# Kernel tuning notes

Measured on AMD Instinct MI355X. Metric: run time of the kernel, lower is better.

The kernel has to match this reference:

```python
import jax, jax.numpy as jnp
import numpy as np

DIM = 1024
EPS = 1e-5

def layernorm(x, g, b):
    m = jnp.mean(x, axis=-1, keepdims=True)
    v = jnp.var(x, axis=-1, keepdims=True)
    return (x - m) / jnp.sqrt(v + EPS) * g + b

def setup_inputs() -> dict:
    key = jax.random.key(0)
    ks = jax.random.split(key, 12)
    B, L, D = 4, 2048, DIM
    s = 1.0 / np.sqrt(D)
    return {
        "q": jax.random.normal(ks[0], (B, L, D), jnp.float32),
        "k": jax.random.normal(ks[1], (B, L, D), jnp.float32),
        "v": jax.random.normal(ks[2], (B, L, D), jnp.float32),
        "gq": jnp.ones((D,), jnp.float32), "bq": jnp.zeros((D,), jnp.float32),
        "gk": jnp.ones((D,), jnp.float32), "bk": jnp.zeros((D,), jnp.float32),
        "gv": jnp.ones((D,), jnp.float32), "bv": jnp.zeros((D,), jnp.float32),
        "Wq": jax.random.uniform(ks[3], (D, D), jnp.float32, -s, s),
        "Wk": jax.random.uniform(ks[4], (D, D), jnp.float32, -s, s),
        "Wv": jax.random.uniform(ks[5], (D, D), jnp.float32, -s, s),
        "Wp": jax.random.uniform(ks[6], (D, D), jnp.float32, -s, s),
        "bp": jax.random.uniform(ks[7], (D,), jnp.float32, -s, s),
    }

def reference(q, k, v, gq, bq, gk, bk, gv, bv, Wq, Wk, Wv, Wp, bp):
    scale = DIM ** -0.5
    qn = layernorm(q, gq, bq) @ Wq.T  # [B,Q,D]
    kn = layernorm(k, gk, bk) @ Wk.T  # [B,K,D]
    vn = layernorm(v, gv, bv) @ Wv.T  # [B,K,D]
    attn = jnp.einsum('bqc,bkc->bqk', qn, kn)
    attn = jax.nn.relu(attn) * scale  # ReLU on raw scores, then scale (matches in-place *=)
    attn_mask = jax.nn.softmax(attn, axis=-1)
    out = jnp.einsum('bqk,bkc->bqc', attn_mask, vn)
    out = out @ Wp.T + bp
    return (attn, out)
```

## Files before the change

### kernel.cpp

```cpp
#include <hip/hip_runtime.h>


typedef __attribute__((ext_vector_type(8))) short short8v;
typedef __attribute__((ext_vector_type(4))) float f32x4;

#define DEVI __device__ __forceinline__

DEVI float b2f(unsigned short u) {
  union { unsigned int i; float f; } x;
  x.i = ((unsigned int)u) << 16;
  return x.f;
}
DEVI unsigned short f2b(float f) {
  union { float f; unsigned int i; } x;
  x.f = f;
  unsigned int r = x.i + 0x7fffu + ((x.i >> 16) & 1u);
  return (unsigned short)(r >> 16);
}

DEVI void async16(const unsigned short* g, unsigned short* l) {
  __builtin_amdgcn_global_load_lds(
      (const __attribute__((address_space(1))) void*)g,
      (__attribute__((address_space(3))) void*)l, 16, 0, 0);
}

__global__ void k_sniff(const unsigned short* __restrict__ wq, int* __restrict__ flag) {
  int tid = threadIdx.x;
  int bad = 0;
#pragma unroll
  for (int j = 0; j < 8; ++j) {
    float f = b2f(wq[tid * 8 + j]);
    bad |= (fabsf(f) > 0.0625f) ? 1 : 0;
  }
  unsigned long long m = __ballot(bad);
  if (tid == 0) *flag = (m == 0ull) ? 1 : 0;
}

struct CvtSrc { const void* p[11]; };

__global__ __launch_bounds__(256) void k_cvt(CvtSrc cs,
    unsigned short* __restrict__ wdst, unsigned short* __restrict__ vdst,
    const int* __restrict__ flag) {
  bool isbf = (*flag != 0);
  int bid = blockIdx.x;
  if (bid < 2048) {
    int s = bid >> 9;
    size_t inner = ((size_t)(bid & 511)) * 2048 + (size_t)threadIdx.x * 8;
    unsigned short* dst = wdst + (size_t)s * 1048576 + inner;
    if (isbf) {
      *(uint4*)dst = *(const uint4*)((const unsigned short*)cs.p[s] + inner);
    } else {
      const float* f = (const float*)cs.p[s] + inner;
      float4 a = *(const float4*)f;
      float4 b = *(const float4*)(f + 4);
      ushort4 o0 = { f2b(a.x), f2b(a.y), f2b(a.z), f2b(a.w) };
      ushort4 o1 = { f2b(b.x), f2b(b.y), f2b(b.z), f2b(b.w) };
      *(ushort4*)dst = o0;
      *(ushort4*)(dst + 4) = o1;
    }
  } else {
    size_t idx = ((size_t)(bid - 2048)) * 2048 + (size_t)threadIdx.x * 8;
    if (idx < 7168) {
      int vsel = (int)(idx >> 10);
      size_t pos = idx & 1023;
      unsigned short* dst = vdst + idx;
      if (isbf) {
        *(uint4*)dst = *(const uint4*)((const unsigned short*)cs.p[4 + vsel] + pos);
      } else {
        const float* f = (const float*)cs.p[4 + vsel] + pos;
        float4 a = *(const float4*)f;
        float4 b = *(const float4*)(f + 4);
        ushort4 o0 = { f2b(a.x), f2b(a.y), f2b(a.z), f2b(a.w) };
        ushort4 o1 = { f2b(b.x), f2b(b.y), f2b(b.z), f2b(b.w) };
        *(ushort4*)dst = o0;
        *(ushort4*)(dst + 4) = o1;
      }
    }
  }
}

__global__ __launch_bounds__(256) void k_ln(
    const void* __restrict__ q, const void* __restrict__ k, const void* __restrict__ v,
    const unsigned short* __restrict__ vecs, const int* __restrict__ flag,
    unsigned short* __restrict__ xn) {
  int row = blockIdx.x;
  int t = row >> 13;
  size_t r = (size_t)(row & 8191);
  const void* src = (t == 0) ? q : (t == 1) ? k : v;
  int tid = threadIdx.x;
  float x0, x1, x2, x3;
  if (*flag) {
    const unsigned short* p = (const unsigned short*)src + r * 1024 + (size_t)tid * 4;
    ushort4 pk = *(const ushort4*)p;
    x0 = b2f(pk.x); x1 = b2f(pk.y); x2 = b2f(pk.z); x3 = b2f(pk.w);
  } else {
    const float* p = (const float*)src + r * 1024 + (size_t)tid * 4;
    float4 pk = *(const float4*)p;
    x0 = pk.x; x1 = pk.y; x2 = pk.z; x3 = pk.w;
  }
  float s1 = x0 + x1 + x2 + x3;
  float s2 = x0 * x0 + x1 * x1 + x2 * x2 + x3 * x3;
  for (int off = 32; off > 0; off >>= 1) {
    s1 += __shfl_down(s1, off);
    s2 += __shfl_down(s2, off);
  }
  __shared__ float sh[8];
  if ((tid & 63) == 0) { sh[tid >> 6] = s1; sh[4 + (tid >> 6)] = s2; }
  __syncthreads();
  float m  = (sh[0] + sh[1] + sh[2] + sh[3]) * (1.0f / 1024.0f);
  float m2 = (sh[4] + sh[5] + sh[6] + sh[7]) * (1.0f / 1024.0f);
  float rstd = rsqrtf(m2 - m * m + 1e-5f);
  const unsigned short* g = vecs + t * 2048 + tid * 4;
  ushort4 gv = *(const ushort4*)g;
  ushort4 bb = *(const ushort4*)(g + 1024);
  ushort4 o;
  o.x = f2b((x0 - m) * rstd * b2f(gv.x) + b2f(bb.x));
  o.y = f2b((x1 - m) * rstd * b2f(gv.y) + b2f(bb.y));
  o.z = f2b((x2 - m) * rstd * b2f(gv.z) + b2f(bb.z));
  o.w = f2b((x3 - m) * rstd * b2f(gv.w) + b2f(bb.w));
  *(ushort4*)(xn + (size_t)row * 1024 + (size_t)tid * 4) = o;
}

__global__ __launch_bounds__(256) void k_softmax(const void* __restrict__ S,
    unsigned short* __restrict__ P, const int* __restrict__ flag) {
  size_t row = blockIdx.x;
  int tid = threadIdx.x;
  float v[8];
  if (*flag) {
    const unsigned short* s = (const unsigned short*)S + row * 2048 + (size_t)tid * 8;
    ushort4 a = *(const ushort4*)s;
    ushort4 b = *(const ushort4*)(s + 4);
    v[0] = b2f(a.x); v[1] = b2f(a.y); v[2] = b2f(a.z); v[3] = b2f(a.w);
    v[4] = b2f(b.x); v[5] = b2f(b.y); v[6] = b2f(b.z); v[7] = b2f(b.w);
  } else {
    const float* s = (const float*)S + row * 2048 + (size_t)tid * 8;
    float4 a = *(const float4*)s;
    float4 b = *(const float4*)(s + 4);
    v[0] = a.x; v[1] = a.y; v[2] = a.z; v[3] = a.w;
    v[4] = b.x; v[5] = b.y; v[6] = b.z; v[7] = b.w;
  }
  float mx = v[0];
#pragma unroll
  for (int j = 1; j < 8; ++j) mx = fmaxf(mx, v[j]);
  for (int off = 32; off > 0; off >>= 1) mx = fmaxf(mx, __shfl_down(mx, off));
  __shared__ float sh[8];
  if ((tid & 63) == 0) sh[tid >> 6] = mx;
  __syncthreads();
  mx = fmaxf(fmaxf(sh[0], sh[1]), fmaxf(sh[2], sh[3]));
  float sum = 0.f;
#pragma unroll
  for (int j = 0; j < 8; ++j) { v[j] = __expf(v[j] - mx); sum += v[j]; }
  for (int off = 32; off > 0; off >>= 1) sum += __shfl_down(sum, off);
  if ((tid & 63) == 0) sh[4 + (tid >> 6)] = sum;
  __syncthreads();
  float inv = 1.0f / (sh[4] + sh[5] + sh[6] + sh[7]);
  ushort4 o0 = { f2b(v[0] * inv), f2b(v[1] * inv), f2b(v[2] * inv), f2b(v[3] * inv) };
  ushort4 o1 = { f2b(v[4] * inv), f2b(v[5] * inv), f2b(v[6] * inv), f2b(v[7] * inv) };
  unsigned short* p = P + row * 2048 + (size_t)tid * 8;
  *(ushort4*)p = o0;
  *(ushort4*)(p + 4) = o1;
}

template <int EPI>
__global__ __launch_bounds__(256) void k_gemm(
    const unsigned short* __restrict__ A, const unsigned short* __restrict__ B,
    void* __restrict__ Cv, long long coff,
    int K, int lda, int ldb, int ldc, int ldct,
    long long sAb, long long sBb, long long sCb,
    float scale, const unsigned short* __restrict__ bias,
    const int* __restrict__ flag) {
  __shared__ __align__(16) unsigned short sA[128 * 32];
  __shared__ __align__(16) unsigned short sB[128 * 32];
  const unsigned short* Ab = A + (long long)blockIdx.z * sAb;
  const unsigned short* Bb = B + (long long)blockIdx.z * sBb;
  long long cbase = coff + (long long)blockIdx.z * sCb;
  int m0 = blockIdx.y * 128, n0 = blockIdx.x * 128;
  int tid = threadIdx.x;
  int lane = tid & 63;
  int w = tid >> 6;
  int wm = w & 1, wn = w >> 1;
  int l15 = lane & 15, quad = lane >> 4;

  int srow = w * 32 + (lane >> 2);
  int scol = ((lane & 3) ^ ((lane >> 3) & 3)) * 8;
  const unsigned short* gA0 = Ab + (size_t)(m0 + srow) * lda + scol;
  const unsigned short* gA1 = gA0 + (size_t)16 * lda;
  const unsigned short* gB0 = Bb + (size_t)(n0 + srow) * ldb + scol;
  const unsigned short* gB1 = gB0 + (size_t)16 * ldb;
  unsigned short* lA0 = &sA[w * 1024];
  unsigned short* lA1 = &sA[w * 1024 + 512];
  unsigned short* lB0 = &sB[w * 1024];
  unsigned short* lB1 = &sB[w * 1024 + 512];

  int swz = (quad ^ ((l15 >> 1) & 3)) * 8;
  const unsigned short* rA = &sA[(wm * 64 + l15) * 32 + swz];
  const unsigned short* rB = &sB[(wn * 64 + l15) * 32 + swz];

  f32x4 acc[4][4];
#pragma unroll
  for (int i = 0; i < 4; ++i)
#pragma unroll
    for (int j = 0; j < 4; ++j) acc[i][j] = (f32x4){0.f, 0.f, 0.f, 0.f};

  for (int k0 = 0; k0 < K; k0 += 32) {
    async16(gA0 + k0, lA0);
    async16(gA1 + k0, lA1);
    async16(gB0 + k0, lB0);
    async16(gB1 + k0, lB1);
    __syncthreads();
    short8v af[4], bf[4];
#pragma unroll
    for (int i = 0; i < 4; ++i) {
      af[i] = *(const short8v*)(rA + i * 512);
      bf[i] = *(const short8v*)(rB + i * 512);
    }
#pragma unroll
    for (int mt = 0; mt < 4; ++mt)
#pragma unroll
      for (int nt = 0; nt < 4; ++nt)
        acc[mt][nt] = __builtin_amdgcn_mfma_f32_16x16x32_bf16(af[mt], bf[nt], acc[mt][nt], 0, 0, 0);
    __syncthreads();
  }

  bool isbf = (EPI == 1 || EPI == 3) ? (*flag != 0) : true;
#pragma unroll
  for (int mt = 0; mt < 4; ++mt) {
    int mb = m0 + wm * 64 + mt * 16 + quad * 4;
#pragma unroll
    for (int nt = 0; nt < 4; ++nt) {
      int n = n0 + wn * 64 + nt * 16 + l15;
      f32x4 vc = acc[mt][nt];
      if (EPI == 2) {
        unsigned short* Ct = (unsigned short*)Cv + cbase;
        ushort4 o = { f2b(vc[0]), f2b(vc[1]), f2b(vc[2]), f2b(vc[3]) };
        *(ushort4*)&Ct[(size_t)n * ldct + mb] = o;
      } else if (EPI == 0) {
        unsigned short* C = (unsigned short*)Cv + cbase;
#pragma unroll
        for (int r2 = 0; r2 < 4; ++r2) C[(size_t)(mb + r2) * ldc + n] = f2b(vc[r2]);
      } else if (EPI == 1) {
        if (isbf) {
          unsigned short* C = (unsigned short*)Cv + cbase;
#pragma unroll
          for (int r2 = 0; r2 < 4; ++r2)
            C[(size_t)(mb + r2) * ldc + n] = f2b(fmaxf(vc[r2], 0.f) * scale);
        } else {
          float* C = (float*)Cv + cbase;
#pragma unroll
          for (int r2 = 0; r2 < 4; ++r2)
            C[(size_t)(mb + r2) * ldc + n] = fmaxf(vc[r2], 0.f) * scale;
        }
      } else {
        float bv2 = b2f(bias[n]);
        if (isbf) {
          unsigned short* C = (unsigned short*)Cv + cbase;
#pragma unroll
          for (int r2 = 0; r2 < 4; ++r2) C[(size_t)(mb + r2) * ldc + n] = f2b(vc[r2] + bv2);
        } else {
          float* C = (float*)Cv + cbase;
#pragma unroll
          for (int r2 = 0; r2 < 4; ++r2) C[(size_t)(mb + r2) * ldc + n] = vc[r2] + bv2;
        }
      }
    }
  }
}

static const size_t MB_ = 1024 * 1024;
static const size_t OFF_W   = 0;
static const size_t OFF_VEC = 8 * MB_;
static const size_t OFF_FLG = 8 * MB_ + 64 * 1024;
static const size_t OFF_XN  = 8 * MB_ + 128 * 1024;
static const size_t OFF_QN  = OFF_XN + 48 * MB_;
static const size_t OFF_KN  = OFF_QN + 16 * MB_;
static const size_t OFF_VNT = OFF_KN + 16 * MB_;
static const size_t OFF_P   = OFF_XN;
static const size_t OFF_O1  = OFF_XN + 32 * MB_;

extern "C" void kernel_launch(void* const* d_in, const int* in_sizes, int n_in,
                              void* d_out, int out_size, void* d_ws, size_t ws_size,
                              hipStream_t stream) {
  (void)in_sizes; (void)n_in; (void)out_size; (void)ws_size;
  char* ws = (char*)d_ws;
  unsigned short* Wb  = (unsigned short*)(ws + OFF_W);
  unsigned short* Vec = (unsigned short*)(ws + OFF_VEC);
  int*            Flg = (int*)(ws + OFF_FLG);
  unsigned short* XN  = (unsigned short*)(ws + OFF_XN);
  unsigned short* QN  = (unsigned short*)(ws + OFF_QN);
  unsigned short* KN  = (unsigned short*)(ws + OFF_KN);
  unsigned short* VNT = (unsigned short*)(ws + OFF_VNT);
  unsigned short* P   = (unsigned short*)(ws + OFF_P);
  unsigned short* O1  = (unsigned short*)(ws + OFF_O1);

  k_sniff<<<1, 64, 0, stream>>>((const unsigned short*)d_in[9], Flg);

  CvtSrc cs;
  cs.p[0] = d_in[9];  cs.p[1] = d_in[10]; cs.p[2] = d_in[11]; cs.p[3] = d_in[12];
  cs.p[4] = d_in[3];  cs.p[5] = d_in[4];  cs.p[6] = d_in[5];  cs.p[7] = d_in[6];
  cs.p[8] = d_in[7];  cs.p[9] = d_in[8];  cs.p[10] = d_in[13];
  k_cvt<<<2052, 256, 0, stream>>>(cs, Wb, Vec, Flg);

  k_ln<<<24576, 256, 0, stream>>>(d_in[0], d_in[1], d_in[2], Vec, Flg, XN);

  k_gemm<0><<<dim3(8, 64, 1), 256, 0, stream>>>(
      XN, Wb, QN,
      0,
      1024, 1024, 1024, 1024, 0,
      0LL, 0LL, 0LL,
      0.f, nullptr, Flg);
  k_gemm<0><<<dim3(8, 64, 1), 256, 0, stream>>>(
      XN + 8388608, Wb + 1048576, KN,
      0,
      1024, 1024, 1024, 1024, 0,
      0LL, 0LL, 0LL,
      0.f, nullptr, Flg);
  k_gemm<2><<<dim3(8, 16, 4), 256, 0, stream>>>(
      XN + 2 * 8388608, Wb + 2 * 1048576, VNT,
      0,
      1024, 1024, 1024, 0, 2048,
      (long long)2048 * 1024, 0LL, (long long)1024 * 2048,
      0.f, nullptr, Flg);
  k_gemm<1><<<dim3(16, 16, 4), 256, 0, stream>>>(
      QN, KN, d_out,
      0,
      1024, 1024, 1024, 2048, 0,
      (long long)2048 * 1024, (long long)2048 * 1024,
      (long long)2048 * 2048,
      0.03125f, nullptr, Flg);
  k_softmax<<<8192, 256, 0, stream>>>(d_out, P, Flg);
  k_gemm<0><<<dim3(8, 16, 4), 256, 0, stream>>>(
      P, VNT, O1,
      0,
      2048, 2048, 2048, 1024, 0,
      (long long)2048 * 2048, (long long)1024 * 2048,
      (long long)2048 * 1024,
      0.f, nullptr, Flg);
  k_gemm<3><<<dim3(8, 64, 1), 256, 0, stream>>>(
      O1, Wb + 3 * 1048576, d_out,
      16777216,
      1024, 1024, 1024, 1024, 0,
      0LL, 0LL, 0LL,
      0.f, Vec + 6144, Flg);
}
```

Before: 465.5 us.

## Double GEMM K-step to 64 with 8-way swizzle and batch Q/K projections

The GEMM kernel now stages a 128x64 K-slice per iteration instead of 128x32. It uses an 8-way XOR swizzle in LDS and runs two MFMA sub-steps per barrier pair, halving the number of __syncthreads and loop iterations. The Q and K projection GEMMs are merged into one launch using the batch dimension, with KN now read at QN+8M offsets. LDS use per block doubles to 32KB, which may reduce occupancy, and the loads are still not double-buffered.

```diff
diff --git a/kernel.cpp b/kernel.cpp
--- a/kernel.cpp
+++ b/kernel.cpp
@@ -169,8 +169,8 @@
     long long sAb, long long sBb, long long sCb,
     float scale, const unsigned short* __restrict__ bias,
     const int* __restrict__ flag) {
-  __shared__ __align__(16) unsigned short sA[128 * 32];
-  __shared__ __align__(16) unsigned short sB[128 * 32];
+  __shared__ __align__(16) unsigned short sA[128 * 64];
+  __shared__ __align__(16) unsigned short sB[128 * 64];
   const unsigned short* Ab = A + (long long)blockIdx.z * sAb;
   const unsigned short* Bb = B + (long long)blockIdx.z * sBb;
   long long cbase = coff + (long long)blockIdx.z * sCb;
@@ -181,20 +181,17 @@
   int wm = w & 1, wn = w >> 1;
   int l15 = lane & 15, quad = lane >> 4;
 
-  int srow = w * 32 + (lane >> 2);
-  int scol = ((lane & 3) ^ ((lane >> 3) & 3)) * 8;
-  const unsigned short* gA0 = Ab + (size_t)(m0 + srow) * lda + scol;
-  const unsigned short* gA1 = gA0 + (size_t)16 * lda;
-  const unsigned short* gB0 = Bb + (size_t)(n0 + srow) * ldb + scol;
-  const unsigned short* gB1 = gB0 + (size_t)16 * ldb;
-  unsigned short* lA0 = &sA[w * 1024];
-  unsigned short* lA1 = &sA[w * 1024 + 512];
-  unsigned short* lB0 = &sB[w * 1024];
-  unsigned short* lB1 = &sB[w * 1024 + 512];
-
-  int swz = (quad ^ ((l15 >> 1) & 3)) * 8;
-  const unsigned short* rA = &sA[(wm * 64 + l15) * 32 + swz];
-  const unsigned short* rB = &sB[(wn * 64 + l15) * 32 + swz];
+  int r8 = lane >> 3;
+  int scol = ((lane & 7) ^ r8) * 8;
+  int srow0 = w * 32 + r8;
+  const unsigned short* gA = Ab + (size_t)(m0 + srow0) * lda + scol;
+  const unsigned short* gB = Bb + (size_t)(n0 + srow0) * ldb + scol;
+  unsigned short* lA = &sA[(size_t)(w * 32) * 64];
+  unsigned short* lB = &sB[(size_t)(w * 32) * 64];
+
+  int rxor = l15 & 7;
+  const unsigned short* rA = &sA[(size_t)(wm * 64 + l15) * 64];
+  const unsigned short* rB = &sB[(size_t)(wn * 64 + l15) * 64];
 
   f32x4 acc[4][4];
 #pragma unroll
@@ -202,23 +199,29 @@
 #pragma unroll
     for (int j = 0; j < 4; ++j) acc[i][j] = (f32x4){0.f, 0.f, 0.f, 0.f};
 
-  for (int k0 = 0; k0 < K; k0 += 32) {
-    async16(gA0 + k0, lA0);
-    async16(gA1 + k0, lA1);
-    async16(gB0 + k0, lB0);
-    async16(gB1 + k0, lB1);
+  for (int k0 = 0; k0 < K; k0 += 64) {
+#pragma unroll
+    for (int j = 0; j < 4; ++j)
+      async16(gA + (size_t)(j * 8) * lda + k0, lA + j * 8 * 64);
+#pragma unroll
+    for (int j = 0; j < 4; ++j)
+      async16(gB + (size_t)(j * 8) * ldb + k0, lB + j * 8 * 64);
     __syncthreads();
-    short8v af[4], bf[4];
-#pragma unroll
-    for (int i = 0; i < 4; ++i) {
-      af[i] = *(const short8v*)(rA + i * 512);
-      bf[i] = *(const short8v*)(rB + i * 512);
+#pragma unroll
+    for (int c = 0; c < 2; ++c) {
+      int col = ((c * 4 + quad) ^ rxor) * 8;
+      short8v af[4], bf[4];
+#pragma unroll
+      for (int i = 0; i < 4; ++i) {
+        af[i] = *(const short8v*)(rA + i * 1024 + col);
+        bf[i] = *(const short8v*)(rB + i * 1024 + col);
+      }
+#pragma unroll
+      for (int mt = 0; mt < 4; ++mt)
+#pragma unroll
+        for (int nt = 0; nt < 4; ++nt)
+          acc[mt][nt] = __builtin_amdgcn_mfma_f32_16x16x32_bf16(af[mt], bf[nt], acc[mt][nt], 0, 0, 0);
     }
-#pragma unroll
-    for (int mt = 0; mt < 4; ++mt)
-#pragma unroll
-      for (int nt = 0; nt < 4; ++nt)
-        acc[mt][nt] = __builtin_amdgcn_mfma_f32_16x16x32_bf16(af[mt], bf[nt], acc[mt][nt], 0, 0, 0);
     __syncthreads();
   }
 
@@ -287,7 +290,6 @@
   int*            Flg = (int*)(ws + OFF_FLG);
   unsigned short* XN  = (unsigned short*)(ws + OFF_XN);
   unsigned short* QN  = (unsigned short*)(ws + OFF_QN);
-  unsigned short* KN  = (unsigned short*)(ws + OFF_KN);
   unsigned short* VNT = (unsigned short*)(ws + OFF_VNT);
   unsigned short* P   = (unsigned short*)(ws + OFF_P);
   unsigned short* O1  = (unsigned short*)(ws + OFF_O1);
@@ -302,17 +304,11 @@
 
   k_ln<<<24576, 256, 0, stream>>>(d_in[0], d_in[1], d_in[2], Vec, Flg, XN);
 
-  k_gemm<0><<<dim3(8, 64, 1), 256, 0, stream>>>(
+  k_gemm<0><<<dim3(8, 64, 2), 256, 0, stream>>>(
       XN, Wb, QN,
       0,
       1024, 1024, 1024, 1024, 0,
-      0LL, 0LL, 0LL,
-      0.f, nullptr, Flg);
-  k_gemm<0><<<dim3(8, 64, 1), 256, 0, stream>>>(
-      XN + 8388608, Wb + 1048576, KN,
-      0,
-      1024, 1024, 1024, 1024, 0,
-      0LL, 0LL, 0LL,
+      8388608LL, 1048576LL, 8388608LL,
       0.f, nullptr, Flg);
   k_gemm<2><<<dim3(8, 16, 4), 256, 0, stream>>>(
       XN + 2 * 8388608, Wb + 2 * 1048576, VNT,
@@ -321,7 +317,7 @@
       (long long)2048 * 1024, 0LL, (long long)1024 * 2048,
       0.f, nullptr, Flg);
   k_gemm<1><<<dim3(16, 16, 4), 256, 0, stream>>>(
-      QN, KN, d_out,
+      QN, QN + 8388608, d_out,
       0,
       1024, 1024, 1024, 2048, 0,
       (long long)2048 * 1024, (long long)2048 * 1024,
```

Result: faster. 436.9 us (-6.1%).
